# Kernel tuning notes

Measured on AMD Instinct MI355X. Metric: run time of the kernel, lower is better.

## Reference

```python
import jax, jax.numpy as jnp
import numpy as np

# SNNConfig constants (see init_kwargs)
TAU_MEM = 0.02
TAU_SYN = 0.005
DT = 0.001
THRESHOLD = 1.0
BETA = 10.0  # fast-sigmoid surrogate beta

BATCH, TIME, IN_DIM, HIDDEN = 32, 1024, 512, 512


@jax.custom_vjp
def spike_fn(v):
    """Heaviside spike with fast-sigmoid surrogate gradient."""
    return (v > THRESHOLD).astype(v.dtype)


def _spike_fwd(v):
    return spike_fn(v), v


def _spike_bwd(v, g):
    x = v - THRESHOLD
    surr = 1.0 / jnp.square(1.0 + BETA * jnp.abs(x))
    return (g * surr,)


spike_fn.defvjp(_spike_fwd, _spike_bwd)


def setup_inputs() -> dict:
    key = jax.random.key(0)
    k1, k2 = jax.random.split(key)
    spikes = jax.random.uniform(k1, (BATCH, TIME, IN_DIM), dtype=jnp.float32)
    # xavier_uniform for (IN_DIM, HIDDEN)
    limit = np.sqrt(6.0 / (IN_DIM + HIDDEN))
    W = jax.random.uniform(k2, (IN_DIM, HIDDEN), dtype=jnp.float32,
                           minval=-limit, maxval=limit)
    b = jnp.zeros((HIDDEN,), dtype=jnp.float32)
    return {"spikes": spikes, "W": W, "b": b}


def reference(spikes, W, b):
    # spikes: [B, T, I]; W: [I, H]; b: [H]
    alpha_mem = jnp.exp(jnp.asarray(-DT / TAU_MEM, dtype=spikes.dtype))
    alpha_syn = jnp.exp(jnp.asarray(-DT / TAU_SYN, dtype=spikes.dtype))
    # hoist the per-step GEMM into one big contraction: [B, T, H]
    I_in = jnp.einsum('bti,ih->bth', spikes, W) + b

    B, T, H = I_in.shape
    v0 = jnp.zeros((B, H), dtype=spikes.dtype)
    s0 = jnp.zeros((B, H), dtype=spikes.dtype)

    def lif_step(carry, i_t):
        v_mem, i_syn = carry
        i_syn = alpha_syn * i_syn + i_t
        v_mem = alpha_mem * v_mem + i_syn
        out = spike_fn(v_mem)
        v_mem = v_mem - out * THRESHOLD  # soft reset
        return (v_mem, i_syn), out

    _, out_spikes = jax.lax.scan(lif_step, (v0, s0), I_in.transpose(1, 0, 2))
    return out_spikes.transpose(1, 0, 2)  # [B, T, H]
```

## Files before the change

kernel.cpp:

```cpp
#include <hip/hip_runtime.h>
#include <hip/hip_bf16.h>

constexpr int BATCH  = 32;
constexpr int TIME   = 1024;
constexpr int IN_DIM = 512;
constexpr int HIDDEN = 512;

constexpr int GM = BATCH * TIME;
constexpr int GN = HIDDEN;
constexpr int GK = IN_DIM;

#define GLOBAL_AS __attribute__((address_space(1)))
#define LDS_AS    __attribute__((address_space(3)))

#define WAITCNT_VMCNT(n) (((n) & 15) | (((n) >> 4) << 14) | (0x7 << 4) | (0xF << 8))

constexpr int BM = 128;
constexpr int BN = 128;
constexpr int BK = 16;
constexpr int LDAs = BM + 4;
constexpr int LDBs = BN + 4;

__global__ __launch_bounds__(256) void sgemm_bias_kernel(
    const float* __restrict__ A,
    const float* __restrict__ B,
    const float* __restrict__ bias,
    float* __restrict__ C)
{
    __shared__ __align__(16) float As[BK * LDAs];
    __shared__ __align__(16) float Bs[BK * LDBs];

    const int tid = threadIdx.x;
    const int bm  = blockIdx.x * BM;
    const int bn  = blockIdx.y * BN;

    const int w    = tid >> 6;
    const int lane = tid & 63;
    const int row0 = (w >> 1) * 64 + (lane >> 3) * 8;
    const int col0 = (w & 1)  * 64 + (lane & 7)  * 8;

    const int ar0 = tid >> 2;
    const int ac  = (tid & 3) << 2;
    const int br0 = tid >> 5;
    const int bc  = (tid & 31) << 2;

    float acc[8][8];
    #pragma unroll
    for (int i = 0; i < 8; ++i)
        #pragma unroll
        for (int j = 0; j < 8; ++j) acc[i][j] = 0.0f;

    #pragma unroll 1
    for (int k0 = 0; k0 < GK; k0 += BK) {
        float4 va0 = *reinterpret_cast<const float4*>(A + (size_t)(bm + ar0) * GK + k0 + ac);
        float4 va1 = *reinterpret_cast<const float4*>(A + (size_t)(bm + ar0 + 64) * GK + k0 + ac);
        float4 vb0 = *reinterpret_cast<const float4*>(B + (size_t)(k0 + br0) * GN + bn + bc);
        float4 vb1 = *reinterpret_cast<const float4*>(B + (size_t)(k0 + br0 + 8) * GN + bn + bc);

        __syncthreads();

        As[(ac + 0) * LDAs + ar0] = va0.x;
        As[(ac + 1) * LDAs + ar0] = va0.y;
        As[(ac + 2) * LDAs + ar0] = va0.z;
        As[(ac + 3) * LDAs + ar0] = va0.w;
        As[(ac + 0) * LDAs + ar0 + 64] = va1.x;
        As[(ac + 1) * LDAs + ar0 + 64] = va1.y;
        As[(ac + 2) * LDAs + ar0 + 64] = va1.z;
        As[(ac + 3) * LDAs + ar0 + 64] = va1.w;
        *reinterpret_cast<float4*>(&Bs[br0 * LDBs + bc]) = vb0;
        *reinterpret_cast<float4*>(&Bs[(br0 + 8) * LDBs + bc]) = vb1;

        __syncthreads();

        #pragma unroll
        for (int kk = 0; kk < BK; ++kk) {
            const float4 a0 = *reinterpret_cast<const float4*>(&As[kk * LDAs + row0]);
            const float4 a1 = *reinterpret_cast<const float4*>(&As[kk * LDAs + row0 + 4]);
            const float4 b0 = *reinterpret_cast<const float4*>(&Bs[kk * LDBs + col0]);
            const float4 b1 = *reinterpret_cast<const float4*>(&Bs[kk * LDBs + col0 + 4]);
            const float arr[8] = {a0.x, a0.y, a0.z, a0.w, a1.x, a1.y, a1.z, a1.w};
            const float brr[8] = {b0.x, b0.y, b0.z, b0.w, b1.x, b1.y, b1.z, b1.w};
            #pragma unroll
            for (int i = 0; i < 8; ++i)
                #pragma unroll
                for (int j = 0; j < 8; ++j)
                    acc[i][j] = fmaf(arr[i], brr[j], acc[i][j]);
        }
    }

    #pragma unroll
    for (int i = 0; i < 8; ++i) {
        const size_t r = (size_t)(bm + row0 + i);
        #pragma unroll
        for (int j = 0; j < 8; j += 4) {
            float4 v;
            v.x = __fadd_rn(acc[i][j + 0], bias[bn + col0 + j + 0]);
            v.y = __fadd_rn(acc[i][j + 1], bias[bn + col0 + j + 1]);
            v.z = __fadd_rn(acc[i][j + 2], bias[bn + col0 + j + 2]);
            v.w = __fadd_rn(acc[i][j + 3], bias[bn + col0 + j + 3]);
            *reinterpret_cast<float4*>(&C[r * GN + bn + col0 + j]) = v;
        }
    }
}

constexpr int SCH    = 32;
constexpr int NCHK   = TIME / SCH;
constexpr int RING_T = 512;
constexpr int RINGC  = RING_T / SCH;

__global__ __launch_bounds__(128) void lif_scan_kernel(
    const float* __restrict__ I,
    float* __restrict__ O)
{
    __shared__ float ring[RING_T * 64];
    __shared__ int prod_c;
    __shared__ int cons_c;

    const int blk  = blockIdx.x;
    const int b    = blk >> 3;
    const int h0   = (blk & 7) * 64;
    const int wave = threadIdx.x >> 6;
    const int lane = threadIdx.x & 63;
    const size_t base = (size_t)b * TIME * HIDDEN + h0;

    if (threadIdx.x == 0) { prod_c = 0; cons_c = 0; }
    __syncthreads();

    if (wave == 0) {
        const float* g0 = I + base + lane;
        #pragma unroll 1
        for (int c = 0; c < NCHK; ++c) {
            if (c >= RINGC) {
                while (__hip_atomic_load(&cons_c, __ATOMIC_ACQUIRE,
                                         __HIP_MEMORY_SCOPE_WORKGROUP)
                       <= c - RINGC) { }
            }
            const int slot = (c & (RINGC - 1)) * SCH;
            #pragma unroll
            for (int u = 0; u < SCH; ++u) {
                const int t = c * SCH + u;
                __builtin_amdgcn_global_load_lds(
                    (GLOBAL_AS const void*)(g0 + (size_t)t * HIDDEN),
                    (LDS_AS void*)&ring[(slot + u) * 64], 4, 0, 0);
            }
            __builtin_amdgcn_s_waitcnt(WAITCNT_VMCNT(32));
            __hip_atomic_store(&prod_c, c, __ATOMIC_RELEASE,
                               __HIP_MEMORY_SCOPE_WORKGROUP);
        }
        __builtin_amdgcn_s_waitcnt(WAITCNT_VMCNT(0));
        __hip_atomic_store(&prod_c, NCHK, __ATOMIC_RELEASE,
                           __HIP_MEMORY_SCOPE_WORKGROUP);
    } else {
        const float am = 0.95122942450071400910f;
        const float as = 0.81873075307798185867f;
        float v = 0.0f, s = 0.0f;
        float* o0 = O + base + lane;

        #pragma unroll 1
        for (int c = 0; c < NCHK; ++c) {
            while (__hip_atomic_load(&prod_c, __ATOMIC_ACQUIRE,
                                     __HIP_MEMORY_SCOPE_WORKGROUP) < c + 1) { }
            const int slot = (c & (RINGC - 1)) * SCH;
            float ob[SCH];
            #pragma unroll
            for (int u = 0; u < SCH; ++u) {
                const float x = ring[(slot + u) * 64 + lane];
                s = __fadd_rn(__fmul_rn(as, s), x);
                v = __fadd_rn(__fmul_rn(am, v), s);
                const float o = (v > 1.0f) ? 1.0f : 0.0f;
                v = __fsub_rn(v, o);
                ob[u] = o;
            }
            #pragma unroll
            for (int u = 0; u < SCH; ++u)
                o0[(size_t)(c * SCH + u) * HIDDEN] = ob[u];
            __hip_atomic_store(&cons_c, c + 1, __ATOMIC_RELEASE,
                               __HIP_MEMORY_SCOPE_WORKGROUP);
        }
    }
}

extern "C" void kernel_launch(void* const* d_in, const int* in_sizes, int n_in,
                              void* d_out, int out_size, void* d_ws, size_t ws_size,
                              hipStream_t stream) {
    const float* spikes = (const float*)d_in[0];
    const float* W      = (const float*)d_in[1];
    const float* bias   = (const float*)d_in[2];
    float* out  = (float*)d_out;
    float* I_in = (float*)d_ws;

    dim3 g1(GM / BM, GN / BN);
    sgemm_bias_kernel<<<g1, 256, 0, stream>>>(spikes, W, bias, I_in);

    lif_scan_kernel<<<BATCH * HIDDEN / 64, 128, 0, stream>>>(I_in, out);
}
```

Measured before the change: 308.2 us.

## Fuse GEMM and LIF scan into one persistent kernel with per-tile flags

Merges the SGEMM and the LIF scan into one launch. GEMM blocks publish a completion flag per output tile, and scan blocks spin on those flags chunk by chunk, so the scan can start on early tiles while the GEMM is still running. The scan ring shrinks from 16 chunks to 2 so it fits in the GEMM's shared memory, and the scan now loads each chunk into registers and writes outputs inside the loop. This risks deadlock if scan blocks are scheduled before the GEMM blocks they wait on. It also adds a flag-zeroing launch and gives scan blocks 256 threads of which 128 exit, which can lower occupancy.

```diff
diff --git a/kernel.cpp b/kernel.cpp
--- a/kernel.cpp
+++ b/kernel.cpp
@@ -1,5 +1,4 @@
 #include <hip/hip_runtime.h>
-#include <hip/hip_bf16.h>
 
 constexpr int BATCH  = 32;
 constexpr int TIME   = 1024;
@@ -21,119 +20,151 @@
 constexpr int LDAs = BM + 4;
 constexpr int LDBs = BN + 4;
 
-__global__ __launch_bounds__(256) void sgemm_bias_kernel(
+constexpr int NGEMM_M = GM / BM;
+constexpr int NGEMM_N = GN / BN;
+constexpr int NGEMM   = NGEMM_M * NGEMM_N;
+constexpr int NSCAN   = BATCH * (HIDDEN/64);
+
+constexpr int SCH   = 32;
+constexpr int NCHK  = TIME / SCH;
+constexpr int RINGC = 2;
+
+static_assert(RINGC * SCH * 64 <= BK * LDAs + BK * LDBs, "ring must fit GEMM smem");
+
+__device__ int g_flags[NGEMM];
+
+__global__ void zero_flags_kernel() {
+    const int i = blockIdx.x * 256 + (int)threadIdx.x;
+    if (i < NGEMM) g_flags[i] = 0;
+}
+
+__global__ __launch_bounds__(256) void fused_kernel(
     const float* __restrict__ A,
     const float* __restrict__ B,
     const float* __restrict__ bias,
-    float* __restrict__ C)
-{
-    __shared__ __align__(16) float As[BK * LDAs];
-    __shared__ __align__(16) float Bs[BK * LDBs];
-
-    const int tid = threadIdx.x;
-    const int bm  = blockIdx.x * BM;
-    const int bn  = blockIdx.y * BN;
-
-    const int w    = tid >> 6;
-    const int lane = tid & 63;
-    const int row0 = (w >> 1) * 64 + (lane >> 3) * 8;
-    const int col0 = (w & 1)  * 64 + (lane & 7)  * 8;
-
-    const int ar0 = tid >> 2;
-    const int ac  = (tid & 3) << 2;
-    const int br0 = tid >> 5;
-    const int bc  = (tid & 31) << 2;
-
-    float acc[8][8];
-    #pragma unroll
-    for (int i = 0; i < 8; ++i)
-        #pragma unroll
-        for (int j = 0; j < 8; ++j) acc[i][j] = 0.0f;
-
-    #pragma unroll 1
-    for (int k0 = 0; k0 < GK; k0 += BK) {
-        float4 va0 = *reinterpret_cast<const float4*>(A + (size_t)(bm + ar0) * GK + k0 + ac);
-        float4 va1 = *reinterpret_cast<const float4*>(A + (size_t)(bm + ar0 + 64) * GK + k0 + ac);
-        float4 vb0 = *reinterpret_cast<const float4*>(B + (size_t)(k0 + br0) * GN + bn + bc);
-        float4 vb1 = *reinterpret_cast<const float4*>(B + (size_t)(k0 + br0 + 8) * GN + bn + bc);
-
-        __syncthreads();
-
-        As[(ac + 0) * LDAs + ar0] = va0.x;
-        As[(ac + 1) * LDAs + ar0] = va0.y;
-        As[(ac + 2) * LDAs + ar0] = va0.z;
-        As[(ac + 3) * LDAs + ar0] = va0.w;
-        As[(ac + 0) * LDAs + ar0 + 64] = va1.x;
-        As[(ac + 1) * LDAs + ar0 + 64] = va1.y;
-        As[(ac + 2) * LDAs + ar0 + 64] = va1.z;
-        As[(ac + 3) * LDAs + ar0 + 64] = va1.w;
-        *reinterpret_cast<float4*>(&Bs[br0 * LDBs + bc]) = vb0;
-        *reinterpret_cast<float4*>(&Bs[(br0 + 8) * LDBs + bc]) = vb1;
-
-        __syncthreads();
-
-        #pragma unroll
-        for (int kk = 0; kk < BK; ++kk) {
-            const float4 a0 = *reinterpret_cast<const float4*>(&As[kk * LDAs + row0]);
-            const float4 a1 = *reinterpret_cast<const float4*>(&As[kk * LDAs + row0 + 4]);
-            const float4 b0 = *reinterpret_cast<const float4*>(&Bs[kk * LDBs + col0]);
-            const float4 b1 = *reinterpret_cast<const float4*>(&Bs[kk * LDBs + col0 + 4]);
-            const float arr[8] = {a0.x, a0.y, a0.z, a0.w, a1.x, a1.y, a1.z, a1.w};
-            const float brr[8] = {b0.x, b0.y, b0.z, b0.w, b1.x, b1.y, b1.z, b1.w};
-            #pragma unroll
-            for (int i = 0; i < 8; ++i)
-                #pragma unroll
-                for (int j = 0; j < 8; ++j)
-                    acc[i][j] = fmaf(arr[i], brr[j], acc[i][j]);
-        }
-    }
-
-    #pragma unroll
-    for (int i = 0; i < 8; ++i) {
-        const size_t r = (size_t)(bm + row0 + i);
-        #pragma unroll
-        for (int j = 0; j < 8; j += 4) {
-            float4 v;
-            v.x = __fadd_rn(acc[i][j + 0], bias[bn + col0 + j + 0]);
-            v.y = __fadd_rn(acc[i][j + 1], bias[bn + col0 + j + 1]);
-            v.z = __fadd_rn(acc[i][j + 2], bias[bn + col0 + j + 2]);
-            v.w = __fadd_rn(acc[i][j + 3], bias[bn + col0 + j + 3]);
-            *reinterpret_cast<float4*>(&C[r * GN + bn + col0 + j]) = v;
-        }
-    }
-}
-
-constexpr int SCH    = 32;
-constexpr int NCHK   = TIME / SCH;
-constexpr int RING_T = 512;
-constexpr int RINGC  = RING_T / SCH;
-
-__global__ __launch_bounds__(128) void lif_scan_kernel(
-    const float* __restrict__ I,
+    float* __restrict__ I_in,
     float* __restrict__ O)
 {
-    __shared__ float ring[RING_T * 64];
+    __shared__ __align__(16) float smem[BK * LDAs + BK * LDBs];
     __shared__ int prod_c;
     __shared__ int cons_c;
 
-    const int blk  = blockIdx.x;
-    const int b    = blk >> 3;
-    const int h0   = (blk & 7) * 64;
+    if (blockIdx.x < (unsigned)NGEMM) {
+        float* As = smem;
+        float* Bs = smem + BK * LDAs;
+
+        const int g   = blockIdx.x;
+        const int tid = threadIdx.x;
+        const int bm  = (g & (NGEMM_M - 1)) * BM;
+        const int bn  = (g >> 8) * BN;
+
+        const int w    = tid >> 6;
+        const int lane = tid & 63;
+        const int row0 = (w >> 1) * 64 + (lane >> 3) * 8;
+        const int col0 = (w & 1)  * 64 + (lane & 7)  * 8;
+
+        const int ar0 = tid >> 2;
+        const int ac  = (tid & 3) << 2;
+        const int br0 = tid >> 5;
+        const int bc  = (tid & 31) << 2;
+
+        float acc[8][8];
+        #pragma unroll
+        for (int i = 0; i < 8; ++i)
+            #pragma unroll
+            for (int j = 0; j < 8; ++j) acc[i][j] = 0.0f;
+
+        #pragma unroll 1
+        for (int k0 = 0; k0 < GK; k0 += BK) {
+            float4 va0 = *reinterpret_cast<const float4*>(A + (size_t)(bm + ar0) * GK + k0 + ac);
+            float4 va1 = *reinterpret_cast<const float4*>(A + (size_t)(bm + ar0 + 64) * GK + k0 + ac);
+            float4 vb0 = *reinterpret_cast<const float4*>(B + (size_t)(k0 + br0) * GN + bn + bc);
+            float4 vb1 = *reinterpret_cast<const float4*>(B + (size_t)(k0 + br0 + 8) * GN + bn + bc);
+
+            __syncthreads();
+
+            As[(ac + 0) * LDAs + ar0] = va0.x;
+            As[(ac + 1) * LDAs + ar0] = va0.y;
+            As[(ac + 2) * LDAs + ar0] = va0.z;
+            As[(ac + 3) * LDAs + ar0] = va0.w;
+            As[(ac + 0) * LDAs + ar0 + 64] = va1.x;
+            As[(ac + 1) * LDAs + ar0 + 64] = va1.y;
+            As[(ac + 2) * LDAs + ar0 + 64] = va1.z;
+            As[(ac + 3) * LDAs + ar0 + 64] = va1.w;
+            *reinterpret_cast<float4*>(&Bs[br0 * LDBs + bc]) = vb0;
+            *reinterpret_cast<float4*>(&Bs[(br0 + 8) * LDBs + bc]) = vb1;
+
+            __syncthreads();
+
+            #pragma unroll
+            for (int kk = 0; kk < BK; ++kk) {
+                const float4 a0 = *reinterpret_cast<const float4*>(&As[kk * LDAs + row0]);
+                const float4 a1 = *reinterpret_cast<const float4*>(&As[kk * LDAs + row0 + 4]);
+                const float4 b0 = *reinterpret_cast<const float4*>(&Bs[kk * LDBs + col0]);
+                const float4 b1 = *reinterpret_cast<const float4*>(&Bs[kk * LDBs + col0 + 4]);
+                const float arr[8] = {a0.x, a0.y, a0.z, a0.w, a1.x, a1.y, a1.z, a1.w};
+                const float brr[8] = {b0.x, b0.y, b0.z, b0.w, b1.x, b1.y, b1.z, b1.w};
+                #pragma unroll
+                for (int i = 0; i < 8; ++i)
+                    #pragma unroll
+                    for (int j = 0; j < 8; ++j)
+                        acc[i][j] = fmaf(arr[i], brr[j], acc[i][j]);
+            }
+        }
+
+        #pragma unroll
+        for (int i = 0; i < 8; ++i) {
+            const size_t r = (size_t)(bm + row0 + i);
+            #pragma unroll
+            for (int j = 0; j < 8; j += 4) {
+                float4 v;
+                v.x = __fadd_rn(acc[i][j + 0], bias[bn + col0 + j + 0]);
+                v.y = __fadd_rn(acc[i][j + 1], bias[bn + col0 + j + 1]);
+                v.z = __fadd_rn(acc[i][j + 2], bias[bn + col0 + j + 2]);
+                v.w = __fadd_rn(acc[i][j + 3], bias[bn + col0 + j + 3]);
+                *reinterpret_cast<float4*>(&I_in[r * GN + bn + col0 + j]) = v;
+            }
+        }
+
+        __syncthreads();
+        if (tid == 0) {
+            __builtin_amdgcn_fence(__ATOMIC_RELEASE, "agent");
+            __hip_atomic_store(&g_flags[g], 1, __ATOMIC_RELAXED,
+                               __HIP_MEMORY_SCOPE_AGENT);
+        }
+        return;
+    }
+
+    if (threadIdx.x == 0) { prod_c = 0; cons_c = 0; }
+    __syncthreads();
+    if (threadIdx.x >= 128) return;
+
+    float* ring = smem;
+
+    const int sb   = (int)blockIdx.x - NGEMM;
+    const int b    = sb >> 3;
+    const int h0   = (sb & 7) * 64;
     const int wave = threadIdx.x >> 6;
     const int lane = threadIdx.x & 63;
     const size_t base = (size_t)b * TIME * HIDDEN + h0;
-
-    if (threadIdx.x == 0) { prod_c = 0; cons_c = 0; }
-    __syncthreads();
+    const int fbase = b * 8 + ((h0 >> 7) << 8);
 
     if (wave == 0) {
-        const float* g0 = I + base + lane;
+        const float* g0 = I_in + base + lane;
         #pragma unroll 1
         for (int c = 0; c < NCHK; ++c) {
+            if ((c & 3) == 0) {
+                const int f = fbase + (c >> 2);
+                while (__hip_atomic_load(&g_flags[f], __ATOMIC_RELAXED,
+                                         __HIP_MEMORY_SCOPE_AGENT) == 0)
+                    __builtin_amdgcn_s_sleep(8);
+                __builtin_amdgcn_fence(__ATOMIC_ACQUIRE, "agent");
+            }
             if (c >= RINGC) {
                 while (__hip_atomic_load(&cons_c, __ATOMIC_ACQUIRE,
                                          __HIP_MEMORY_SCOPE_WORKGROUP)
-                       <= c - RINGC) { }
+                       <= c - RINGC)
+                    __builtin_amdgcn_s_sleep(1);
             }
             const int slot = (c & (RINGC - 1)) * SCH;
             #pragma unroll
@@ -159,21 +190,21 @@
         #pragma unroll 1
         for (int c = 0; c < NCHK; ++c) {
             while (__hip_atomic_load(&prod_c, __ATOMIC_ACQUIRE,
-                                     __HIP_MEMORY_SCOPE_WORKGROUP) < c + 1) { }
+                                     __HIP_MEMORY_SCOPE_WORKGROUP) < c + 1)
+                __builtin_amdgcn_s_sleep(1);
             const int slot = (c & (RINGC - 1)) * SCH;
-            float ob[SCH];
+            float x[SCH];
+            #pragma unroll
+            for (int u = 0; u < SCH; ++u)
+                x[u] = ring[(slot + u) * 64 + lane];
             #pragma unroll
             for (int u = 0; u < SCH; ++u) {
-                const float x = ring[(slot + u) * 64 + lane];
-                s = __fadd_rn(__fmul_rn(as, s), x);
+                s = __fadd_rn(__fmul_rn(as, s), x[u]);
                 v = __fadd_rn(__fmul_rn(am, v), s);
                 const float o = (v > 1.0f) ? 1.0f : 0.0f;
                 v = __fsub_rn(v, o);
-                ob[u] = o;
-            }
-            #pragma unroll
-            for (int u = 0; u < SCH; ++u)
-                o0[(size_t)(c * SCH + u) * HIDDEN] = ob[u];
+                o0[(size_t)(c * SCH + u) * HIDDEN] = o;
+            }
             __hip_atomic_store(&cons_c, c + 1, __ATOMIC_RELEASE,
                                __HIP_MEMORY_SCOPE_WORKGROUP);
         }
@@ -189,8 +220,6 @@
     float* out  = (float*)d_out;
     float* I_in = (float*)d_ws;
 
-    dim3 g1(GM / BM, GN / BN);
-    sgemm_bias_kernel<<<g1, 256, 0, stream>>>(spikes, W, bias, I_in);
-
-    lif_scan_kernel<<<BATCH * HIDDEN / 64, 128, 0, stream>>>(I_in, out);
+    zero_flags_kernel<<<dim3((NGEMM + 255) / 256), 256, 0, stream>>>();
+    fused_kernel<<<dim3(NGEMM + NSCAN), 256, 0, stream>>>(spikes, W, bias, I_in, out);
 }
```

After: 377.7 us. 1.23x slower.

## Replace LDS producer/consumer ring in LIF scan with register double-buffered prefetch

Applied to the files above, without the earlier changes.

The LIF scan kernel drops its two-wave design, where one wave streamed inputs into a 512-step LDS ring and the other consumed them under atomic flag handshakes. It now uses a single wave per block that prefetches the next 32-step chunk into registers while computing the current one, ping-ponging between two register arrays. This removes the spin-wait synchronization and LDS traffic, but the prefetch depth is much shallower (one chunk versus up to sixteen), so memory latency may be less well hidden. With only 256 single-wave blocks, latency hiding rests entirely on in-flight register loads.

```diff
diff --git a/kernel.cpp b/kernel.cpp
--- a/kernel.cpp
+++ b/kernel.cpp
@@ -1,5 +1,4 @@
 #include <hip/hip_runtime.h>
-#include <hip/hip_bf16.h>
 
 constexpr int BATCH  = 32;
 constexpr int TIME   = 1024;
@@ -9,11 +8,6 @@
 constexpr int GM = BATCH * TIME;
 constexpr int GN = HIDDEN;
 constexpr int GK = IN_DIM;
-
-#define GLOBAL_AS __attribute__((address_space(1)))
-#define LDS_AS    __attribute__((address_space(3)))
-
-#define WAITCNT_VMCNT(n) (((n) & 15) | (((n) >> 4) << 14) | (0x7 << 4) | (0xF << 8))
 
 constexpr int BM = 128;
 constexpr int BN = 128;
@@ -103,80 +97,66 @@
     }
 }
 
-constexpr int SCH    = 32;
-constexpr int NCHK   = TIME / SCH;
-constexpr int RING_T = 512;
-constexpr int RINGC  = RING_T / SCH;
+constexpr int SCH  = 32;
+constexpr int NCHK = TIME / SCH;
 
-__global__ __launch_bounds__(128) void lif_scan_kernel(
+__global__ __launch_bounds__(64) void lif_scan_v2(
     const float* __restrict__ I,
     float* __restrict__ O)
 {
-    __shared__ float ring[RING_T * 64];
-    __shared__ int prod_c;
-    __shared__ int cons_c;
-
     const int blk  = blockIdx.x;
     const int b    = blk >> 3;
     const int h0   = (blk & 7) * 64;
-    const int wave = threadIdx.x >> 6;
-    const int lane = threadIdx.x & 63;
-    const size_t base = (size_t)b * TIME * HIDDEN + h0;
+    const int lane = threadIdx.x;
+    const size_t base = (size_t)b * TIME * HIDDEN + h0 + lane;
+    const float* g0 = I + base;
+    float*       o0 = O + base;
 
-    if (threadIdx.x == 0) { prod_c = 0; cons_c = 0; }
-    __syncthreads();
+    const float am = 0.95122942450071400910f;
+    const float as = 0.81873075307798185867f;
+    float v = 0.0f, s = 0.0f;
 
-    if (wave == 0) {
-        const float* g0 = I + base + lane;
-        #pragma unroll 1
-        for (int c = 0; c < NCHK; ++c) {
-            if (c >= RINGC) {
-                while (__hip_atomic_load(&cons_c, __ATOMIC_ACQUIRE,
-                                         __HIP_MEMORY_SCOPE_WORKGROUP)
-                       <= c - RINGC) { }
-            }
-            const int slot = (c & (RINGC - 1)) * SCH;
-            #pragma unroll
-            for (int u = 0; u < SCH; ++u) {
-                const int t = c * SCH + u;
-                __builtin_amdgcn_global_load_lds(
-                    (GLOBAL_AS const void*)(g0 + (size_t)t * HIDDEN),
-                    (LDS_AS void*)&ring[(slot + u) * 64], 4, 0, 0);
-            }
-            __builtin_amdgcn_s_waitcnt(WAITCNT_VMCNT(32));
-            __hip_atomic_store(&prod_c, c, __ATOMIC_RELEASE,
-                               __HIP_MEMORY_SCOPE_WORKGROUP);
+    float xa[SCH], xb[SCH], ob[SCH];
+
+    #pragma unroll
+    for (int u = 0; u < SCH; ++u)
+        xa[u] = g0[(size_t)u * HIDDEN];
+
+    #pragma unroll 1
+    for (int c = 0; c < NCHK; c += 2) {
+        #pragma unroll
+        for (int u = 0; u < SCH; ++u)
+            xb[u] = g0[(size_t)((c + 1) * SCH + u) * HIDDEN];
+
+        #pragma unroll
+        for (int u = 0; u < SCH; ++u) {
+            s = __fadd_rn(__fmul_rn(as, s), xa[u]);
+            v = __fadd_rn(__fmul_rn(am, v), s);
+            const float o = (v > 1.0f) ? 1.0f : 0.0f;
+            v = __fsub_rn(v, o);
+            ob[u] = o;
         }
-        __builtin_amdgcn_s_waitcnt(WAITCNT_VMCNT(0));
-        __hip_atomic_store(&prod_c, NCHK, __ATOMIC_RELEASE,
-                           __HIP_MEMORY_SCOPE_WORKGROUP);
-    } else {
-        const float am = 0.95122942450071400910f;
-        const float as = 0.81873075307798185867f;
-        float v = 0.0f, s = 0.0f;
-        float* o0 = O + base + lane;
+        #pragma unroll
+        for (int u = 0; u < SCH; ++u)
+            o0[(size_t)(c * SCH + u) * HIDDEN] = ob[u];
 
-        #pragma unroll 1
-        for (int c = 0; c < NCHK; ++c) {
-            while (__hip_atomic_load(&prod_c, __ATOMIC_ACQUIRE,
-                                     __HIP_MEMORY_SCOPE_WORKGROUP) < c + 1) { }
-            const int slot = (c & (RINGC - 1)) * SCH;
-            float ob[SCH];
-            #pragma unroll
-            for (int u = 0; u < SCH; ++u) {
-                const float x = ring[(slot + u) * 64 + lane];
-                s = __fadd_rn(__fmul_rn(as, s), x);
-                v = __fadd_rn(__fmul_rn(am, v), s);
-                const float o = (v > 1.0f) ? 1.0f : 0.0f;
-                v = __fsub_rn(v, o);
-                ob[u] = o;
-            }
+        if (c + 2 < NCHK) {
             #pragma unroll
             for (int u = 0; u < SCH; ++u)
-                o0[(size_t)(c * SCH + u) * HIDDEN] = ob[u];
-            __hip_atomic_store(&cons_c, c + 1, __ATOMIC_RELEASE,
-                               __HIP_MEMORY_SCOPE_WORKGROUP);
+                xa[u] = g0[(size_t)((c + 2) * SCH + u) * HIDDEN];
         }
+
+        #pragma unroll
+        for (int u = 0; u < SCH; ++u) {
+            s = __fadd_rn(__fmul_rn(as, s), xb[u]);
+            v = __fadd_rn(__fmul_rn(am, v), s);
+            const float o = (v > 1.0f) ? 1.0f : 0.0f;
+            v = __fsub_rn(v, o);
+            ob[u] = o;
+        }
+        #pragma unroll
+        for (int u = 0; u < SCH; ++u)
+            o0[(size_t)((c + 1) * SCH + u) * HIDDEN] = ob[u];
     }
 }
 
@@ -192,5 +172,5 @@
     dim3 g1(GM / BM, GN / BN);
     sgemm_bias_kernel<<<g1, 256, 0, stream>>>(spikes, W, bias, I_in);
 
-    lif_scan_kernel<<<BATCH * HIDDEN / 64, 128, 0, stream>>>(I_in, out);
+    lif_scan_v2<<<BATCH * HIDDEN / 64, 64, 0, stream>>>(I_in, out);
 }
```

New measurement: 311.8 us. Within noise of the previous version (+1.2%).
